# Kernel tuning notes

Hardware: AMD Instinct MI355X
Metric: run time of the kernel (lower is better)

Reference implementation:

```python
import jax, jax.numpy as jnp
import numpy as np

N_NODES = 50000
N_EDGES = 800000
CHANNELS = 96
STEPS = 10
ALPHA = 0.1


def setup_inputs() -> dict:
    key = jax.random.key(0)
    k1, k2 = jax.random.split(key)
    x = jax.random.normal(k1, (N_NODES, CHANNELS), dtype=jnp.float32)
    edge_index = jax.random.randint(k2, (2, N_EDGES), 0, N_NODES, dtype=jnp.int64)
    # gamma initialized exactly as the module: [alpha*(1-alpha)^k for k<steps] + [(1-alpha)^steps]
    gamma = jnp.asarray(
        [ALPHA * (1.0 - ALPHA) ** k for k in range(STEPS)] + [(1.0 - ALPHA) ** STEPS],
        dtype=jnp.float32,
    )
    return {"x": x, "edge_index": edge_index, "gamma": gamma}


def reference(x, edge_index, gamma):
    # GPR-GNN propagation: H^(0)=x, H^(k)=D^-1/2 A D^-1/2 H^(k-1); out = sum_k gamma_k H^(k)
    n = x.shape[0]
    src, dst = edge_index[0], edge_index[1]
    deg = jax.ops.segment_sum(jnp.ones((src.shape[0],), x.dtype), dst, num_segments=n)
    dinv = jnp.where(deg > 0, jax.lax.rsqrt(jnp.maximum(deg, 1.0)), 0.0).astype(x.dtype)
    norm = (dinv[src] * dinv[dst])[:, None]  # [E, 1]

    def prop(h):
        # gather from src, scale by symmetric norm, scatter-add into dst
        return jax.ops.segment_sum(h[src] * norm, dst, num_segments=n)

    out = gamma[0] * x
    h = x
    for k in range(STEPS):
        h = prop(h)
        out = out + gamma[k + 1] * h
    return out
```

## Files before the change

### kernel.cpp

```cpp
#include <hip/hip_runtime.h>
#include <hip/hip_fp16.h>

#define N_NODES 50000
#define N_EDGES 800000
#define CH 96
#define NSLICE 4
#define CPN 3
#define ROWB 64
#define STEPS 10
#define SENT N_NODES
#define NDST_X 6250

#define SLICE_STRIDE 3200256ull
#define SLAB (4ull * SLICE_STRIDE)


__global__ void count_deg(const int* __restrict__ ei, int* __restrict__ deg, int ne) {
    int xr = blockIdx.x & 7;
    int lo = xr * NDST_X, hi = lo + NDST_X;
    int t = (blockIdx.x >> 3) * 256 + threadIdx.x;
    int e = t * 4;
    if (e < ne) {
        int4 d4 = *(const int4*)(ei + ne + e);
        if (d4.x >= lo && d4.x < hi) atomicAdd(&deg[d4.x], 1);
        if (d4.y >= lo && d4.y < hi) atomicAdd(&deg[d4.y], 1);
        if (d4.z >= lo && d4.z < hi) atomicAdd(&deg[d4.z], 1);
        if (d4.w >= lo && d4.w < hi) atomicAdd(&deg[d4.w], 1);
    }
}

__global__ void scan1(const int* __restrict__ deg, int* __restrict__ row_ptr,
                      int* __restrict__ partials, float* __restrict__ dinv, int n) {
    __shared__ int sm[256];
    int i = blockIdx.x * 256 + threadIdx.x;
    int v = 0;
    if (i < n) {
        int d = deg[i];
        dinv[i] = (d > 0) ? (1.0f / sqrtf((float)d)) : 0.0f;
        v = (d + 3) & ~3;
    }
    sm[threadIdx.x] = v;
    __syncthreads();
    for (int off = 1; off < 256; off <<= 1) {
        int t = (threadIdx.x >= off) ? sm[threadIdx.x - off] : 0;
        __syncthreads();
        sm[threadIdx.x] += t;
        __syncthreads();
    }
    if (i < n) row_ptr[i + 1] = sm[threadIdx.x];
    if (threadIdx.x == 255) partials[blockIdx.x] = sm[255];
}

__global__ void scan2(int* __restrict__ partials, int nb) {
    __shared__ int sm[256];
    int v = (threadIdx.x < nb) ? partials[threadIdx.x] : 0;
    sm[threadIdx.x] = v;
    __syncthreads();
    for (int off = 1; off < 256; off <<= 1) {
        int t = (threadIdx.x >= off) ? sm[threadIdx.x - off] : 0;
        __syncthreads();
        sm[threadIdx.x] += t;
        __syncthreads();
    }
    if (threadIdx.x < nb) partials[threadIdx.x] = sm[threadIdx.x] - v;
}

__global__ void scan3(int* __restrict__ row_ptr, const int* __restrict__ partials, int n) {
    int i = blockIdx.x * 256 + threadIdx.x;
    if (i < n) row_ptr[i + 1] += partials[blockIdx.x];
    if (i == 0) row_ptr[0] = 0;
}

__global__ void pad_fill(const int* __restrict__ deg, const int* __restrict__ row_ptr,
                         unsigned short* __restrict__ cs, int n) {
    int i = blockIdx.x * blockDim.x + threadIdx.x;
    if (i < n) {
        int dg = deg[i];
        int dp = (dg + 3) & ~3;
        int base = row_ptr[i];
        for (int j = dg; j < dp; ++j) cs[base + j] = (unsigned short)SENT;
    }
}

__global__ void fill_csr(const int* __restrict__ ei, const int* __restrict__ row_ptr,
                         int* __restrict__ deg, unsigned short* __restrict__ cs, int ne) {
    int xr = blockIdx.x & 7;
    int lo = xr * NDST_X, hi = lo + NDST_X;
    int t = (blockIdx.x >> 3) * 256 + threadIdx.x;
    int e = t * 4;
    if (e < ne) {
        int4 s4 = *(const int4*)(ei + e);
        int4 d4 = *(const int4*)(ei + ne + e);
        #pragma unroll
        for (int j = 0; j < 4; ++j) {
            int s = (j == 0) ? s4.x : (j == 1) ? s4.y : (j == 2) ? s4.z : s4.w;
            int d = (j == 0) ? d4.x : (j == 1) ? d4.y : (j == 2) ? d4.z : d4.w;
            if (d < lo || d >= hi) continue;
            if ((unsigned)s >= (unsigned)N_NODES) s = SENT;
            int slot = atomicSub(&deg[d], 1) - 1;
            cs[row_ptr[d] + slot] = (unsigned short)s;
        }
    }
}

__global__ __launch_bounds__(256) void prescale16(const float* __restrict__ x,
                                                  const float* __restrict__ dinv,
                                                  char* __restrict__ p0) {
    int slice = blockIdx.x & 3;
    int t = (blockIdx.x >> 2) * 256 + threadIdx.x;
    if (t >= N_NODES * CPN) return;
    int node = t / CPN;
    int chunk = t - node * CPN;
    float dv = dinv[node];
    const float4* xb = (const float4*)((const char*)x + (size_t)node * 384 + slice * 96 + chunk * 32);
    float4 x0 = xb[0], x1 = xb[1];
    uint4 q;
    ((__half2*)&q)[0] = __floats2half2_rn(dv * x0.x, dv * x0.y);
    ((__half2*)&q)[1] = __floats2half2_rn(dv * x0.z, dv * x0.w);
    ((__half2*)&q)[2] = __floats2half2_rn(dv * x1.x, dv * x1.y);
    ((__half2*)&q)[3] = __floats2half2_rn(dv * x1.z, dv * x1.w);
    *(uint4*)(p0 + (size_t)slice * SLICE_STRIDE + (size_t)node * ROWB + chunk * 16) = q;
}

__global__ void zero_sent(char* __restrict__ p_base, int nbuf) {
    int t = blockIdx.x * blockDim.x + threadIdx.x;
    if (t < nbuf * NSLICE * CPN) {
        int chunk = t % CPN;
        int slice = (t / CPN) % NSLICE;
        int buf   = t / (CPN * NSLICE);
        uint4 z = {0u, 0u, 0u, 0u};
        *(uint4*)(p_base + (size_t)buf * SLAB + (size_t)slice * SLICE_STRIDE
                  + (size_t)SENT * ROWB + chunk * 16) = z;
    }
}

__device__ inline void acc8(float* a, uint4 q) {
    const __half2* h = (const __half2*)&q;
    #pragma unroll
    for (int i = 0; i < 4; ++i) {
        float2 f = __half22float2(h[i]);
        a[2 * i] += f.x; a[2 * i + 1] += f.y;
    }
}

__global__ __launch_bounds__(256) void prop16(const char* __restrict__ pin_slab,
                                              char* __restrict__ pout_slab,
                                              float* __restrict__ out,
                                              const float* __restrict__ x,
                                              const int* __restrict__ row_ptr,
                                              const unsigned short* __restrict__ cs,
                                              const float* __restrict__ dinv,
                                              const float* __restrict__ gamma, int k) {
    int slice = blockIdx.x & 3;
    int t = (blockIdx.x >> 2) * 256 + threadIdx.x;
    if (t >= N_NODES * CPN) return;
    int node = t / CPN;
    int chunk = t - node * CPN;
    const char* pin = pin_slab + (size_t)slice * SLICE_STRIDE + chunk * 16;
    int beg = row_ptr[node];
    int end = row_ptr[node + 1];

    float acc[8] = {0.f, 0.f, 0.f, 0.f, 0.f, 0.f, 0.f, 0.f};

    for (int e = beg; e < end; e += 4) {
        ushort4 m = *(const ushort4*)(cs + e);
        uint4 q0 = *(const uint4*)(pin + (size_t)m.x * ROWB);
        uint4 q1 = *(const uint4*)(pin + (size_t)m.y * ROWB);
        uint4 q2 = *(const uint4*)(pin + (size_t)m.z * ROWB);
        uint4 q3 = *(const uint4*)(pin + (size_t)m.w * ROWB);
        acc8(acc, q0);
        acc8(acc, q1);
        acc8(acc, q2);
        acc8(acc, q3);
    }

    float dv = dinv[node];

    if (pout_slab) {
        float s = dv * dv;
        uint4 q;
        ((__half2*)&q)[0] = __floats2half2_rn(s * acc[0], s * acc[1]);
        ((__half2*)&q)[1] = __floats2half2_rn(s * acc[2], s * acc[3]);
        ((__half2*)&q)[2] = __floats2half2_rn(s * acc[4], s * acc[5]);
        ((__half2*)&q)[3] = __floats2half2_rn(s * acc[6], s * acc[7]);
        *(uint4*)(pout_slab + (size_t)slice * SLICE_STRIDE + (size_t)node * ROWB + chunk * 16) = q;
    }

    if (out) {
        float gk = gamma[k + 1] * dv;
        float4* ob = (float4*)((char*)out + (size_t)node * 384 + slice * 96 + chunk * 32);
        float4 o0, o1;
        if (k == 0) {
            float g0 = gamma[0];
            const float4* xb = (const float4*)((const char*)x + (size_t)node * 384 + slice * 96 + chunk * 32);
            float4 x0 = xb[0], x1 = xb[1];
            o0.x = fmaf(gk, acc[0], g0 * x0.x); o0.y = fmaf(gk, acc[1], g0 * x0.y);
            o0.z = fmaf(gk, acc[2], g0 * x0.z); o0.w = fmaf(gk, acc[3], g0 * x0.w);
            o1.x = fmaf(gk, acc[4], g0 * x1.x); o1.y = fmaf(gk, acc[5], g0 * x1.y);
            o1.z = fmaf(gk, acc[6], g0 * x1.z); o1.w = fmaf(gk, acc[7], g0 * x1.w);
        } else {
            o0 = ob[0]; o1 = ob[1];
            o0.x = fmaf(gk, acc[0], o0.x); o0.y = fmaf(gk, acc[1], o0.y);
            o0.z = fmaf(gk, acc[2], o0.z); o0.w = fmaf(gk, acc[3], o0.w);
            o1.x = fmaf(gk, acc[4], o1.x); o1.y = fmaf(gk, acc[5], o1.y);
            o1.z = fmaf(gk, acc[6], o1.z); o1.w = fmaf(gk, acc[7], o1.w);
        }
        ob[0] = o0; ob[1] = o1;
    }
}

__global__ __launch_bounds__(256) void finalize(const char* __restrict__ p_base,
                                                const float* __restrict__ x,
                                                const float* __restrict__ dinv,
                                                const float* __restrict__ gamma,
                                                float* __restrict__ out) {
    int slice = blockIdx.x & 3;
    int t = (blockIdx.x >> 2) * 256 + threadIdx.x;
    if (t >= N_NODES * CPN) return;
    int node = t / CPN;
    int chunk = t - node * CPN;
    float dv  = dinv[node];
    float rdv = (dv > 0.f) ? (1.f / dv) : 0.f;

    const float4* xb = (const float4*)((const char*)x + (size_t)node * 384 + slice * 96 + chunk * 32);
    float4 x0 = xb[0], x1 = xb[1];
    float g0 = gamma[0];
    float o[8] = {g0 * x0.x, g0 * x0.y, g0 * x0.z, g0 * x0.w,
                  g0 * x1.x, g0 * x1.y, g0 * x1.z, g0 * x1.w};

    const char* p = p_base + SLAB + (size_t)slice * SLICE_STRIDE + (size_t)node * ROWB + chunk * 16;
    for (int k = 1; k <= STEPS; ++k) {
        uint4 q = *(const uint4*)p;
        p += SLAB;
        float gk = gamma[k] * rdv;
        const __half2* h = (const __half2*)&q;
        #pragma unroll
        for (int i = 0; i < 4; ++i) {
            float2 f = __half22float2(h[i]);
            o[2 * i]     = fmaf(gk, f.x, o[2 * i]);
            o[2 * i + 1] = fmaf(gk, f.y, o[2 * i + 1]);
        }
    }
    float4* ob = (float4*)((char*)out + (size_t)node * 384 + slice * 96 + chunk * 32);
    ob[0] = make_float4(o[0], o[1], o[2], o[3]);
    ob[1] = make_float4(o[4], o[5], o[6], o[7]);
}


static inline size_t align_up(size_t v, size_t a) { return (v + a - 1) & ~(a - 1); }

extern "C" void kernel_launch(void* const* d_in, const int* in_sizes, int n_in,
                              void* d_out, int out_size, void* d_ws, size_t ws_size,
                              hipStream_t stream) {
    const float* x     = (const float*)d_in[0];
    const int*   ei    = (const int*)d_in[1];
    const float* gamma = (const float*)d_in[2];
    float*       out   = (float*)d_out;

    const int n  = N_NODES;
    const int ne = N_EDGES;
    const int nblk_nodes = (n + 255) / 256;
    const int ne_pad_max = ne + 4 * n;

    char*  ws  = (char*)d_ws;
    size_t off = 0;
    int*   deg      = (int*)(ws + off);   off = align_up(off + (size_t)n * 4, 256);
    int*   row_ptr  = (int*)(ws + off);   off = align_up(off + (size_t)(n + 1) * 4, 256);
    int*   partials = (int*)(ws + off);   off = align_up(off + (size_t)nblk_nodes * 4, 256);
    float* dinv     = (float*)(ws + off); off = align_up(off + (size_t)n * 4, 256);
    unsigned short* cs = (unsigned short*)(ws + off);
    off = align_up(off + (size_t)ne_pad_max * 2, 256);
    char*  p_base   = ws + off;

    const bool deferred = (ws_size >= off + 11ull * SLAB);
    const int  nbuf     = deferred ? 11 : 2;

    (void)hipMemsetAsync(deg, 0, (size_t)n * 4, stream);

    const int nblk_e4 = (ne / 4 + 255) / 256;
    count_deg<<<8 * nblk_e4, 256, 0, stream>>>(ei, deg, ne);

    scan1<<<nblk_nodes, 256, 0, stream>>>(deg, row_ptr, partials, dinv, n);
    scan2<<<1, 256, 0, stream>>>(partials, nblk_nodes);
    scan3<<<nblk_nodes, 256, 0, stream>>>(row_ptr, partials, n);

    pad_fill<<<nblk_nodes, 256, 0, stream>>>(deg, row_ptr, cs, n);
    fill_csr<<<8 * nblk_e4, 256, 0, stream>>>(ei, row_ptr, deg, cs, ne);

    const int nt = n * CPN;
    const int nblk_t = (nt + 255) / 256;
    const int nblk_sl = NSLICE * nblk_t;
    prescale16<<<nblk_sl, 256, 0, stream>>>(x, dinv, p_base);
    zero_sent<<<1, 256, 0, stream>>>(p_base, nbuf);

    if (deferred) {
        for (int k = 0; k < STEPS; ++k) {
            const char* pin  = p_base + (size_t)k * SLAB;
            char*       pout = p_base + (size_t)(k + 1) * SLAB;
            prop16<<<nblk_sl, 256, 0, stream>>>(pin, pout, nullptr, x,
                                                row_ptr, cs, dinv, gamma, k);
        }
        finalize<<<nblk_sl, 256, 0, stream>>>(p_base, x, dinv, gamma, out);
    } else {
        char* pA = p_base;
        char* pB = p_base + SLAB;
        const char* pin = pA;
        char* pout = pB;
        for (int k = 0; k < STEPS; ++k) {
            char* pw = (k == STEPS - 1) ? nullptr : pout;
            prop16<<<nblk_sl, 256, 0, stream>>>(pin, pw, out, x,
                                                row_ptr, cs, dinv, gamma, k);
            pin  = pout;
            pout = (pout == pB) ? pA : pB;
        }
    }
}
```

Before: 449.2 us.

## Repartition features into three 32-channel slices and map slices to XCD groups

Features are now split into three slices of 32 channels, each a full 64-byte fp16 row, with four lanes per node, replacing four slices of 24 channels with three lanes per node. Row gathers now use the whole 64-byte slot instead of 48 of 64 bytes, which cuts the total gather traffic. The prop kernel's block-to-slice mapping assigns XCDs 0-2, 3-5 and 6-7 to slices 0, 1 and 2, so each slice's gather working set stays in fewer L2 caches. The 3/3/2 XCD split is uneven, so XCDs 6-7 carry more work per die and some blocks of the rounded grid exit early.

```diff
diff --git a/kernel.cpp b/kernel.cpp
--- a/kernel.cpp
+++ b/kernel.cpp
@@ -4,15 +4,19 @@
 #define N_NODES 50000
 #define N_EDGES 800000
 #define CH 96
-#define NSLICE 4
-#define CPN 3
+#define NSLICE 3
+#define SUBS 4
 #define ROWB 64
 #define STEPS 10
 #define SENT N_NODES
 #define NDST_X 6250
-
-#define SLICE_STRIDE 3200256ull
-#define SLAB (4ull * SLICE_STRIDE)
+#define LANES_PER_SLICE (N_NODES * SUBS)
+#define NBLK_SLICE 782
+#define PROP_ROUNDS 391
+#define PROP_GRID (PROP_ROUNDS * 8)
+
+#define SLICE3 3200256ull
+#define SLAB (3ull * SLICE3)
 
 
 __global__ void count_deg(const int* __restrict__ ei, int* __restrict__ deg, int ne) {
@@ -106,31 +110,32 @@
 __global__ __launch_bounds__(256) void prescale16(const float* __restrict__ x,
                                                   const float* __restrict__ dinv,
                                                   char* __restrict__ p0) {
-    int slice = blockIdx.x & 3;
-    int t = (blockIdx.x >> 2) * 256 + threadIdx.x;
-    if (t >= N_NODES * CPN) return;
-    int node = t / CPN;
-    int chunk = t - node * CPN;
+    int idx = blockIdx.x * 256 + threadIdx.x;
+    if (idx >= NSLICE * LANES_PER_SLICE) return;
+    int slice = idx / LANES_PER_SLICE;
+    int rem   = idx - slice * LANES_PER_SLICE;
+    int node  = rem >> 2;
+    int sub   = rem & 3;
     float dv = dinv[node];
-    const float4* xb = (const float4*)((const char*)x + (size_t)node * 384 + slice * 96 + chunk * 32);
+    const float4* xb = (const float4*)((const char*)x + (size_t)node * 384 + slice * 128 + sub * 32);
     float4 x0 = xb[0], x1 = xb[1];
     uint4 q;
     ((__half2*)&q)[0] = __floats2half2_rn(dv * x0.x, dv * x0.y);
     ((__half2*)&q)[1] = __floats2half2_rn(dv * x0.z, dv * x0.w);
     ((__half2*)&q)[2] = __floats2half2_rn(dv * x1.x, dv * x1.y);
     ((__half2*)&q)[3] = __floats2half2_rn(dv * x1.z, dv * x1.w);
-    *(uint4*)(p0 + (size_t)slice * SLICE_STRIDE + (size_t)node * ROWB + chunk * 16) = q;
+    *(uint4*)(p0 + (size_t)slice * SLICE3 + (size_t)node * ROWB + sub * 16) = q;
 }
 
 __global__ void zero_sent(char* __restrict__ p_base, int nbuf) {
-    int t = blockIdx.x * blockDim.x + threadIdx.x;
-    if (t < nbuf * NSLICE * CPN) {
-        int chunk = t % CPN;
-        int slice = (t / CPN) % NSLICE;
-        int buf   = t / (CPN * NSLICE);
+    int t = blockIdx.x * 256 + threadIdx.x;
+    if (t < nbuf * NSLICE * SUBS) {
+        int sub   = t & 3;
+        int slice = (t >> 2) % NSLICE;
+        int buf   = t / (SUBS * NSLICE);
         uint4 z = {0u, 0u, 0u, 0u};
-        *(uint4*)(p_base + (size_t)buf * SLAB + (size_t)slice * SLICE_STRIDE
-                  + (size_t)SENT * ROWB + chunk * 16) = z;
+        *(uint4*)(p_base + (size_t)buf * SLAB + (size_t)slice * SLICE3
+                  + (size_t)SENT * ROWB + sub * 16) = z;
     }
 }
 
@@ -151,12 +156,20 @@
                                               const unsigned short* __restrict__ cs,
                                               const float* __restrict__ dinv,
                                               const float* __restrict__ gamma, int k) {
-    int slice = blockIdx.x & 3;
-    int t = (blockIdx.x >> 2) * 256 + threadIdx.x;
-    if (t >= N_NODES * CPN) return;
-    int node = t / CPN;
-    int chunk = t - node * CPN;
-    const char* pin = pin_slab + (size_t)slice * SLICE_STRIDE + chunk * 16;
+    int xcd = blockIdx.x & 7;
+    int r   = blockIdx.x >> 3;
+    int slice, pos, gsz;
+    if (xcd < 3)      { slice = 0; pos = xcd;     gsz = 3; }
+    else if (xcd < 6) { slice = 1; pos = xcd - 3; gsz = 3; }
+    else              { slice = 2; pos = xcd - 6; gsz = 2; }
+    int lb = r * gsz + pos;
+    if (lb >= NBLK_SLICE) return;
+    int t = lb * 256 + threadIdx.x;
+    if (t >= LANES_PER_SLICE) return;
+    int node = t >> 2;
+    int sub  = t & 3;
+
+    const char* pin = pin_slab + (size_t)slice * SLICE3 + sub * 16;
     int beg = row_ptr[node];
     int end = row_ptr[node + 1];
 
@@ -183,16 +196,16 @@
         ((__half2*)&q)[1] = __floats2half2_rn(s * acc[2], s * acc[3]);
         ((__half2*)&q)[2] = __floats2half2_rn(s * acc[4], s * acc[5]);
         ((__half2*)&q)[3] = __floats2half2_rn(s * acc[6], s * acc[7]);
-        *(uint4*)(pout_slab + (size_t)slice * SLICE_STRIDE + (size_t)node * ROWB + chunk * 16) = q;
+        *(uint4*)(pout_slab + (size_t)slice * SLICE3 + (size_t)node * ROWB + sub * 16) = q;
     }
 
     if (out) {
         float gk = gamma[k + 1] * dv;
-        float4* ob = (float4*)((char*)out + (size_t)node * 384 + slice * 96 + chunk * 32);
+        float4* ob = (float4*)((char*)out + (size_t)node * 384 + slice * 128 + sub * 32);
         float4 o0, o1;
         if (k == 0) {
             float g0 = gamma[0];
-            const float4* xb = (const float4*)((const char*)x + (size_t)node * 384 + slice * 96 + chunk * 32);
+            const float4* xb = (const float4*)((const char*)x + (size_t)node * 384 + slice * 128 + sub * 32);
             float4 x0 = xb[0], x1 = xb[1];
             o0.x = fmaf(gk, acc[0], g0 * x0.x); o0.y = fmaf(gk, acc[1], g0 * x0.y);
             o0.z = fmaf(gk, acc[2], g0 * x0.z); o0.w = fmaf(gk, acc[3], g0 * x0.w);
@@ -214,21 +227,22 @@
                                                 const float* __restrict__ dinv,
                                                 const float* __restrict__ gamma,
                                                 float* __restrict__ out) {
-    int slice = blockIdx.x & 3;
-    int t = (blockIdx.x >> 2) * 256 + threadIdx.x;
-    if (t >= N_NODES * CPN) return;
-    int node = t / CPN;
-    int chunk = t - node * CPN;
+    int idx = blockIdx.x * 256 + threadIdx.x;
+    if (idx >= NSLICE * LANES_PER_SLICE) return;
+    int slice = idx / LANES_PER_SLICE;
+    int rem   = idx - slice * LANES_PER_SLICE;
+    int node  = rem >> 2;
+    int sub   = rem & 3;
     float dv  = dinv[node];
     float rdv = (dv > 0.f) ? (1.f / dv) : 0.f;
 
-    const float4* xb = (const float4*)((const char*)x + (size_t)node * 384 + slice * 96 + chunk * 32);
+    const float4* xb = (const float4*)((const char*)x + (size_t)node * 384 + slice * 128 + sub * 32);
     float4 x0 = xb[0], x1 = xb[1];
     float g0 = gamma[0];
     float o[8] = {g0 * x0.x, g0 * x0.y, g0 * x0.z, g0 * x0.w,
                   g0 * x1.x, g0 * x1.y, g0 * x1.z, g0 * x1.w};
 
-    const char* p = p_base + SLAB + (size_t)slice * SLICE_STRIDE + (size_t)node * ROWB + chunk * 16;
+    const char* p = p_base + SLAB + (size_t)slice * SLICE3 + (size_t)node * ROWB + sub * 16;
     for (int k = 1; k <= STEPS; ++k) {
         uint4 q = *(const uint4*)p;
         p += SLAB;
@@ -241,7 +255,7 @@
             o[2 * i + 1] = fmaf(gk, f.y, o[2 * i + 1]);
         }
     }
-    float4* ob = (float4*)((char*)out + (size_t)node * 384 + slice * 96 + chunk * 32);
+    float4* ob = (float4*)((char*)out + (size_t)node * 384 + slice * 128 + sub * 32);
     ob[0] = make_float4(o[0], o[1], o[2], o[3]);
     ob[1] = make_float4(o[4], o[5], o[6], o[7]);
 }
@@ -287,20 +301,19 @@
     pad_fill<<<nblk_nodes, 256, 0, stream>>>(deg, row_ptr, cs, n);
     fill_csr<<<8 * nblk_e4, 256, 0, stream>>>(ei, row_ptr, deg, cs, ne);
 
-    const int nt = n * CPN;
-    const int nblk_t = (nt + 255) / 256;
-    const int nblk_sl = NSLICE * nblk_t;
-    prescale16<<<nblk_sl, 256, 0, stream>>>(x, dinv, p_base);
+    const int nlin = NSLICE * LANES_PER_SLICE;
+    const int nblk_lin = (nlin + 255) / 256;
+    prescale16<<<nblk_lin, 256, 0, stream>>>(x, dinv, p_base);
     zero_sent<<<1, 256, 0, stream>>>(p_base, nbuf);
 
     if (deferred) {
         for (int k = 0; k < STEPS; ++k) {
             const char* pin  = p_base + (size_t)k * SLAB;
             char*       pout = p_base + (size_t)(k + 1) * SLAB;
-            prop16<<<nblk_sl, 256, 0, stream>>>(pin, pout, nullptr, x,
-                                                row_ptr, cs, dinv, gamma, k);
-        }
-        finalize<<<nblk_sl, 256, 0, stream>>>(p_base, x, dinv, gamma, out);
+            prop16<<<PROP_GRID, 256, 0, stream>>>(pin, pout, nullptr, x,
+                                                  row_ptr, cs, dinv, gamma, k);
+        }
+        finalize<<<nblk_lin, 256, 0, stream>>>(p_base, x, dinv, gamma, out);
     } else {
         char* pA = p_base;
         char* pB = p_base + SLAB;
@@ -308,8 +321,8 @@
         char* pout = pB;
         for (int k = 0; k < STEPS; ++k) {
             char* pw = (k == STEPS - 1) ? nullptr : pout;
-            prop16<<<nblk_sl, 256, 0, stream>>>(pin, pw, out, x,
-                                                row_ptr, cs, dinv, gamma, k);
+            prop16<<<PROP_GRID, 256, 0, stream>>>(pin, pw, out, x,
+                                                  row_ptr, cs, dinv, gamma, k);
             pin  = pout;
             pout = (pout == pB) ? pA : pB;
         }
```

New measurement: 415.1 us. 1.08x faster.
